# Performance work log

Hardware: AMD Instinct MI355X
Metric: run time of the kernel (lower is better)

## Reference

```python
import jax, jax.numpy as jnp
import numpy as np

N, E, G = 50000, 800000, 512
DIN, HID, DOUT, L, DE = 64, 64, 128, 3, 16
NEG_SLOPE = 0.2
BN_EPS = 1e-5


def setup_inputs() -> dict:
    key = jax.random.key(0)
    ks = jax.random.split(key, 20)
    s = 0.1  # weight scale for numerical stability
    return {
        "x": jax.random.normal(ks[0], (N, DIN), jnp.float32),
        "edge_index": jax.random.randint(ks[1], (2, E), 0, N, jnp.int32),
        "edge_attr": jax.random.normal(ks[2], (E, DE), jnp.float32),
        "batch": jnp.sort(jax.random.randint(ks[3], (N,), 0, G, jnp.int32)),
        "emb_W": jax.random.normal(ks[4], (HID, DIN), jnp.float32) * s,
        "emb_b": jax.random.normal(ks[5], (HID,), jnp.float32) * s,
        "Wl": jax.random.normal(ks[6], (L, HID, HID), jnp.float32) * s,
        "bl": jax.random.normal(ks[7], (L, HID), jnp.float32) * s,
        "Wr": jax.random.normal(ks[8], (L, HID, HID), jnp.float32) * s,
        "br": jax.random.normal(ks[9], (L, HID), jnp.float32) * s,
        "We": jax.random.normal(ks[10], (L, HID, DE), jnp.float32) * s,
        "att": jax.random.normal(ks[11], (L, HID), jnp.float32) * s,
        "conv_bias": jax.random.normal(ks[12], (L, HID), jnp.float32) * s,
        "bn_gamma": jax.random.uniform(ks[13], (L, HID), jnp.float32, 0.5, 1.5),
        "bn_beta": jax.random.normal(ks[14], (L, HID), jnp.float32) * s,
        "bn_mean": jnp.zeros((L, HID), jnp.float32),
        "bn_var": jnp.ones((L, HID), jnp.float32),
        "lin_W": jax.random.normal(ks[15], (DOUT, HID), jnp.float32) * s,
        "lin_b": jax.random.normal(ks[16], (DOUT,), jnp.float32) * s,
    }


def _gatv2(h, src, dst, edge_attr, Wl, bl, Wr, br, We, att, bias):
    # GATv2Conv, heads=1, concat=False, with edge features
    xl = h @ Wl.T + bl                      # [N,C] source transform (also message value)
    xr = h @ Wr.T + br                      # [N,C] target transform
    ea = edge_attr @ We.T                   # [E,C]
    m = xl[src] + xr[dst] + ea              # [E,C]
    m = jax.nn.leaky_relu(m, NEG_SLOPE)
    alpha = m @ att                         # [E] attention logits
    amax = jax.ops.segment_max(alpha, dst, num_segments=N)
    ea_exp = jnp.exp(alpha - amax[dst])
    denom = jax.ops.segment_sum(ea_exp, dst, num_segments=N)
    alpha = ea_exp / (denom[dst] + 1e-16)
    out = jax.ops.segment_sum(alpha[:, None] * xl[src], dst, num_segments=N)
    return out + bias


def reference(x, edge_index, edge_attr, batch, emb_W, emb_b, Wl, bl, Wr, br,
              We, att, conv_bias, bn_gamma, bn_beta, bn_mean, bn_var, lin_W, lin_b):
    src, dst = edge_index[0], edge_index[1]
    h = x @ emb_W.T + emb_b
    for i in range(L):
        hc = _gatv2(h, src, dst, edge_attr, Wl[i], bl[i], Wr[i], br[i],
                    We[i], att[i], conv_bias[i])
        # BatchNorm (eval mode, running stats)
        hc = (hc - bn_mean[i]) * jax.lax.rsqrt(bn_var[i] + BN_EPS) * bn_gamma[i] + bn_beta[i]
        hc = jax.nn.gelu(hc, approximate=False)  # torch F.gelu default is exact erf
        h = h + hc                                # residual; dropout p=0 / eval -> identity
    out = h @ lin_W.T + lin_b                     # [N,DOUT]
    counts = jax.ops.segment_sum(jnp.ones((N,), out.dtype), batch, num_segments=G)
    pooled = jax.ops.segment_sum(out, batch, num_segments=G)
    return pooled / jnp.maximum(counts, 1.0)[:, None]
```

## Files before the change

### kernel.cpp

```cpp
#include <hip/hip_runtime.h>
#include <math.h>

#define NEG_SLOPE 0.2f
#define BN_EPS 1e-5f

template <int N> struct IC { static constexpr int v = N; };
template <bool B> struct BC { static constexpr bool v = B; };

typedef _Float16 half2v __attribute__((ext_vector_type(2)));
typedef _Float16 f16x8 __attribute__((ext_vector_type(8)));
typedef float f32x4v __attribute__((ext_vector_type(4)));

__device__ __forceinline__ half2v u2h(unsigned u) {
  union { unsigned u; half2v h; } c;
  c.u = u;
  return c.h;
}
__device__ __forceinline__ unsigned pkh(float lo, float hi) {
  union { half2v h; unsigned u; } c;
  c.h[0] = (_Float16)lo;
  c.h[1] = (_Float16)hi;
  return c.u;
}

#if defined(__has_builtin)
#if __has_builtin(__builtin_amdgcn_fdot2)
#define FDOT2(a, b, c) __builtin_amdgcn_fdot2((a), (b), (c), false)
#endif
#endif
#ifndef FDOT2
__device__ __forceinline__ float fdot2_sw(half2v a, half2v b, float c) {
  return c + (float)a[0] * (float)b[0] + (float)a[1] * (float)b[1];
}
#define FDOT2(a, b, c) fdot2_sw((a), (b), (c))
#endif

#if defined(__has_builtin)
#if __has_builtin(__builtin_amdgcn_exp2f)
#define FEXP(x) __builtin_amdgcn_exp2f(x)
#define ATT_SCALE 1.44269504088896f
#endif
#endif
#ifndef FEXP
#define FEXP(x) __expf(x)
#define ATT_SCALE 1.0f
#endif

#define FMA4(acc, v, wq) \
  acc += (v).x * (wq).x + (v).y * (wq).y + (v).z * (wq).z + (v).w * (wq).w

#define DOT_ROW(buf, stride, r, bias, OUT)                                  \
  {                                                                         \
    __builtin_amdgcn_sched_barrier(0);                                      \
    float a0 = 0.f, a1 = 0.f, a2 = 0.f, a3 = 0.f;                           \
    _Pragma("unroll") for (int q = 0; q < 4; q++) {                         \
      float4 v0 = *(const float4*)((buf) + (r) * (stride) + q * 16 + 0);    \
      float4 v1 = *(const float4*)((buf) + (r) * (stride) + q * 16 + 4);    \
      float4 v2 = *(const float4*)((buf) + (r) * (stride) + q * 16 + 8);    \
      float4 v3 = *(const float4*)((buf) + (r) * (stride) + q * 16 + 12);   \
      FMA4(a0, v0, W[q * 4 + 0]);                                           \
      FMA4(a1, v1, W[q * 4 + 1]);                                           \
      FMA4(a2, v2, W[q * 4 + 2]);                                           \
      FMA4(a3, v3, W[q * 4 + 3]);                                           \
    }                                                                       \
    OUT = (bias) + ((a0 + a1) + (a2 + a3));                                 \
  }

__device__ __forceinline__ float wave_sum64(float v) {
  int x;
  x = __builtin_amdgcn_update_dpp(0, __float_as_int(v), 0x121, 0xF, 0xF, true);
  v += __int_as_float(x);
  x = __builtin_amdgcn_update_dpp(0, __float_as_int(v), 0x122, 0xF, 0xF, true);
  v += __int_as_float(x);
  x = __builtin_amdgcn_update_dpp(0, __float_as_int(v), 0x124, 0xF, 0xF, true);
  v += __int_as_float(x);
  x = __builtin_amdgcn_update_dpp(0, __float_as_int(v), 0x128, 0xF, 0xF, true);
  v += __int_as_float(x);
  x = __builtin_amdgcn_update_dpp(0, __float_as_int(v), 0x142, 0xF, 0xF, true);
  v += __int_as_float(x);
  x = __builtin_amdgcn_update_dpp(0, __float_as_int(v), 0x143, 0xF, 0xF, true);
  v += __int_as_float(x);
  return __int_as_float(__builtin_amdgcn_readlane(__float_as_int(v), 63));
}

#if defined(__has_builtin)
#if __has_builtin(__builtin_amdgcn_mfma_f32_16x16x32_f16)
#define HAVE_MFMA16 1
#endif
#endif

__global__ __launch_bounds__(256) void hist_kernel(
    const int* __restrict__ dst, const int* __restrict__ batch,
    int* __restrict__ deg, float* __restrict__ counts,
    const float* __restrict__ Wl, const float* __restrict__ Wr,
    _Float16* __restrict__ w16, int E_, int N_) {
  int i = blockIdx.x * 256 + threadIdx.x;
  if (i < E_) atomicAdd(&deg[dst[i]], 1);
  if (i < N_) atomicAdd(&counts[batch[i]], 1.0f);
  if (i < 24576)
    w16[i] = (i < 12288) ? (_Float16)Wl[i] : (_Float16)Wr[i - 12288];
}

__global__ __launch_bounds__(256) void scanA_kernel(
    const int* __restrict__ deg, int* __restrict__ row_ptr,
    int* __restrict__ segTot, int* __restrict__ bins, int N_, int nseg) {
  __shared__ int sb[256];
  __shared__ int lb[128];
  int t = threadIdx.x;
  if (t < 128) lb[t] = 0;
  __syncthreads();
  for (int s = blockIdx.x; s < nseg; s += gridDim.x) {
    int i = s * 256 + t;
    int v = (i < N_) ? deg[i] : 0;
    if (i < N_) atomicAdd(&lb[127 - min(v, 127)], 1);
    sb[t] = v;
    __syncthreads();
    for (int off = 1; off < 256; off <<= 1) {
      int a = (t >= off) ? sb[t - off] : 0;
      __syncthreads();
      sb[t] += a;
      __syncthreads();
    }
    int incl = sb[t];
    if (i < N_) row_ptr[i] = incl - v;
    if (t == 255) segTot[s] = incl;
    __syncthreads();
  }
  if (t < 128 && lb[t]) atomicAdd(&bins[t], lb[t]);
}

__global__ __launch_bounds__(256) void scanB_kernel(int* __restrict__ segTot,
                                                    int* __restrict__ bins,
                                                    int nseg) {
  __shared__ int sb[256];
  __shared__ int baseSh;
  int t = threadIdx.x;
  if (t == 0) baseSh = 0;
  __syncthreads();
  for (int c0 = 0; c0 < nseg; c0 += 256) {
    int s = c0 + t;
    int v = (s < nseg) ? segTot[s] : 0;
    sb[t] = v;
    __syncthreads();
    for (int off = 1; off < 256; off <<= 1) {
      int a = (t >= off) ? sb[t - off] : 0;
      __syncthreads();
      sb[t] += a;
      __syncthreads();
    }
    int incl = sb[t];
    int base = baseSh;
    if (s < nseg) segTot[s] = base + incl - v;
    __syncthreads();
    if (t == 255) baseSh = base + incl;
    __syncthreads();
  }
  int v2 = (t < 128) ? bins[t] : 0;
  sb[t] = v2;
  __syncthreads();
  for (int off = 1; off < 256; off <<= 1) {
    int a = (t >= off) ? sb[t - off] : 0;
    __syncthreads();
    sb[t] += a;
    __syncthreads();
  }
  if (t < 128) bins[t] = sb[t] - v2;
}

__global__ __launch_bounds__(256) void scanC_kernel(
    int* __restrict__ row_ptr, const int* __restrict__ segTot,
    int* __restrict__ cursor, const int* __restrict__ deg,
    int* __restrict__ bins, int* __restrict__ perm, int N_, int E_) {
  __shared__ int lb[128];
  __shared__ int lbase[128];
  int t = threadIdx.x;
  if (t < 128) lb[t] = 0;
  __syncthreads();
  int i = blockIdx.x * 256 + t;
  int bin = 0, rk = 0;
  bool ok = (i < N_);
  if (ok) {
    int rp = row_ptr[i] + segTot[i >> 8];
    row_ptr[i] = rp;
    cursor[i] = rp;
    int dg = deg[i];
    bin = 127 - min(dg, 127);
    rk = atomicAdd(&lb[bin], 1);
  }
  if (i == 0) row_ptr[N_] = E_;
  __syncthreads();
  if (t < 128) {
    int c = lb[t];
    lbase[t] = c ? atomicAdd(&bins[t], c) : 0;
  }
  __syncthreads();
  if (ok) perm[lbase[bin] + rk] = i;
}

__global__ __launch_bounds__(256) void scatter_kernel(
    const int* __restrict__ src, const int* __restrict__ dst,
    int* __restrict__ cursor, int* __restrict__ csr_src,
    int* __restrict__ csr_eid, int E_) {
  int e = blockIdx.x * 256 + threadIdx.x;
  if (e >= E_) return;
  int pos = atomicAdd(&cursor[dst[e]], 1);
  csr_src[pos] = src[e];
  csr_eid[pos] = e;
}

__global__ __launch_bounds__(256) void permute_attr_kernel(
    const float4* __restrict__ edge_attr4, const int* __restrict__ csr_eid,
    unsigned* __restrict__ attr_u, int E_) {
  int p = blockIdx.x * 256 + threadIdx.x;
  if (p >= E_) return;
  int e = csr_eid[p];
  float4 a0 = edge_attr4[(size_t)e * 4 + 0];
  float4 a1 = edge_attr4[(size_t)e * 4 + 1];
  float4 a2 = edge_attr4[(size_t)e * 4 + 2];
  float4 a3 = edge_attr4[(size_t)e * 4 + 3];
  uint4 u0, u1;
  u0.x = pkh(a0.x, a0.y);
  u0.y = pkh(a0.z, a0.w);
  u0.z = pkh(a1.x, a1.y);
  u0.w = pkh(a1.z, a1.w);
  u1.x = pkh(a2.x, a2.y);
  u1.y = pkh(a2.z, a2.w);
  u1.z = pkh(a3.x, a3.y);
  u1.w = pkh(a3.z, a3.w);
  uint4* d4 = (uint4*)(attr_u + (size_t)p * 8);
  d4[0] = u0;
  d4[1] = u1;
}

__global__ __launch_bounds__(256, 3) void emb_kernel(
    const float* __restrict__ x, const float* __restrict__ emb_W,
    const float* __restrict__ emb_b, const _Float16* __restrict__ Wl16,
    const float* __restrict__ bl, const _Float16* __restrict__ Wr16,
    const float* __restrict__ br, float* __restrict__ h,
    _Float16* __restrict__ xl, _Float16* __restrict__ xr, int rows) {
  __shared__ float sx[4096];
  __shared__ float sh[64 * 68];
  int lane = threadIdx.x & 63;
  int w = threadIdx.x >> 6;
  int n0 = blockIdx.x * 64;

  {
    int gmax = rows * 64 - 4;
#pragma unroll
    for (int i = 0; i < 4; i++) {
      int off = w * 1024 + i * 256 + lane * 4;
      int g = min(n0 * 64 + off, gmax);
      *(float4*)(sx + off) = *(const float4*)(x + g);
    }
  }

  {
    float4 W[16];
#pragma unroll
    for (int q = 0; q < 16; q++) W[q] = ((const float4*)(emb_W + lane * 64))[q];
    float b = emb_b[lane];
#pragma unroll 1
    for (int t = 0; t < 16; t++) {
      int r = w * 16 + t;
      float a;
      DOT_ROW(sx, 64, r, b, a);
      sh[r * 68 + lane] = a;
      int n = n0 + r;
      if (n < rows) h[(size_t)n * 64 + lane] = a;
    }
  }

#ifdef HAVE_MFMA16
  {
    int r = lane & 15;
    int kg = lane >> 4;
    int nb = n0 + w * 16;
    const float* p = sh + (w * 16 + r) * 68 + kg * 8;
    f16x8 A0, A1;
    {
      float4 xa = *(const float4*)(p);
      float4 xb = *(const float4*)(p + 4);
      A0[0] = (_Float16)xa.x; A0[1] = (_Float16)xa.y;
      A0[2] = (_Float16)xa.z; A0[3] = (_Float16)xa.w;
      A0[4] = (_Float16)xb.x; A0[5] = (_Float16)xb.y;
      A0[6] = (_Float16)xb.z; A0[7] = (_Float16)xb.w;
      xa = *(const float4*)(p + 32);
      xb = *(const float4*)(p + 36);
      A1[0] = (_Float16)xa.x; A1[1] = (_Float16)xa.y;
      A1[2] = (_Float16)xa.z; A1[3] = (_Float16)xa.w;
      A1[4] = (_Float16)xb.x; A1[5] = (_Float16)xb.y;
      A1[6] = (_Float16)xb.z; A1[7] = (_Float16)xb.w;
    }
#pragma unroll
    for (int c = 0; c < 4; c++) {
      int o = c * 16 + r;
      {
        const f16x8* b0 = (const f16x8*)(Wl16 + (size_t)o * 64 + kg * 8);
        const f16x8* b1 = (const f16x8*)(Wl16 + (size_t)o * 64 + 32 + kg * 8);
        f32x4v acc;
        float bv = bl[o];
        acc[0] = bv; acc[1] = bv; acc[2] = bv; acc[3] = bv;
        acc = __builtin_amdgcn_mfma_f32_16x16x32_f16(A0, b0[0], acc, 0, 0, 0);
        acc = __builtin_amdgcn_mfma_f32_16x16x32_f16(A1, b1[0], acc, 0, 0, 0);
#pragma unroll
        for (int g = 0; g < 4; g++) {
          int nd = nb + kg * 4 + g;
          if (nd < rows) xl[(size_t)nd * 64 + o] = (_Float16)acc[g];
        }
      }
      {
        const f16x8* b0 = (const f16x8*)(Wr16 + (size_t)o * 64 + kg * 8);
        const f16x8* b1 = (const f16x8*)(Wr16 + (size_t)o * 64 + 32 + kg * 8);
        f32x4v acc;
        float bv = br[o];
        acc[0] = bv; acc[1] = bv; acc[2] = bv; acc[3] = bv;
        acc = __builtin_amdgcn_mfma_f32_16x16x32_f16(A0, b0[0], acc, 0, 0, 0);
        acc = __builtin_amdgcn_mfma_f32_16x16x32_f16(A1, b1[0], acc, 0, 0, 0);
#pragma unroll
        for (int g = 0; g < 4; g++) {
          int nd = nb + kg * 4 + g;
          if (nd < rows) xr[(size_t)nd * 64 + o] = (_Float16)acc[g];
        }
      }
    }
  }
#endif
}

__global__ __launch_bounds__(256) void linx_mfma_kernel(
    const float* __restrict__ in, const _Float16* __restrict__ Wl16,
    const float* __restrict__ bl, const _Float16* __restrict__ Wr16,
    const float* __restrict__ br, _Float16* __restrict__ xl,
    _Float16* __restrict__ xr, int rows) {
#ifdef HAVE_MFMA16
  int lane = threadIdx.x & 63;
  int w = threadIdx.x >> 6;
  int n0 = blockIdx.x * 64 + w * 16;
  int r = lane & 15;
  int kg = lane >> 4;

  int nA = min(n0 + r, rows - 1);
  f16x8 A0, A1;
  {
    const float* p = in + (size_t)nA * 64 + kg * 8;
    float4 xa = *(const float4*)(p);
    float4 xb = *(const float4*)(p + 4);
    A0[0] = (_Float16)xa.x; A0[1] = (_Float16)xa.y;
    A0[2] = (_Float16)xa.z; A0[3] = (_Float16)xa.w;
    A0[4] = (_Float16)xb.x; A0[5] = (_Float16)xb.y;
    A0[6] = (_Float16)xb.z; A0[7] = (_Float16)xb.w;
    xa = *(const float4*)(p + 32);
    xb = *(const float4*)(p + 36);
    A1[0] = (_Float16)xa.x; A1[1] = (_Float16)xa.y;
    A1[2] = (_Float16)xa.z; A1[3] = (_Float16)xa.w;
    A1[4] = (_Float16)xb.x; A1[5] = (_Float16)xb.y;
    A1[6] = (_Float16)xb.z; A1[7] = (_Float16)xb.w;
  }

#pragma unroll
  for (int c = 0; c < 4; c++) {
    int o = c * 16 + r;
    {
      const f16x8* b0 = (const f16x8*)(Wl16 + (size_t)o * 64 + kg * 8);
      const f16x8* b1 = (const f16x8*)(Wl16 + (size_t)o * 64 + 32 + kg * 8);
      f32x4v acc;
      float bv = bl[o];
      acc[0] = bv; acc[1] = bv; acc[2] = bv; acc[3] = bv;
      acc = __builtin_amdgcn_mfma_f32_16x16x32_f16(A0, b0[0], acc, 0, 0, 0);
      acc = __builtin_amdgcn_mfma_f32_16x16x32_f16(A1, b1[0], acc, 0, 0, 0);
#pragma unroll
      for (int g = 0; g < 4; g++) {
        int nd = n0 + kg * 4 + g;
        if (nd < rows) xl[(size_t)nd * 64 + o] = (_Float16)acc[g];
      }
    }
    {
      const f16x8* b0 = (const f16x8*)(Wr16 + (size_t)o * 64 + kg * 8);
      const f16x8* b1 = (const f16x8*)(Wr16 + (size_t)o * 64 + 32 + kg * 8);
      f32x4v acc;
      float bv = br[o];
      acc[0] = bv; acc[1] = bv; acc[2] = bv; acc[3] = bv;
      acc = __builtin_amdgcn_mfma_f32_16x16x32_f16(A0, b0[0], acc, 0, 0, 0);
      acc = __builtin_amdgcn_mfma_f32_16x16x32_f16(A1, b1[0], acc, 0, 0, 0);
#pragma unroll
      for (int g = 0; g < 4; g++) {
        int nd = n0 + kg * 4 + g;
        if (nd < rows) xr[(size_t)nd * 64 + o] = (_Float16)acc[g];
      }
    }
  }
#endif
}

template <bool CONTIG>
__global__ __launch_bounds__(256) void gat_fused_kernel(
    const int* __restrict__ perm, const int* __restrict__ csr_src,
    const int* __restrict__ csr_eid, const int* __restrict__ row_ptr,
    const unsigned* __restrict__ attr_u, const float* __restrict__ edge_attr,
    const _Float16* __restrict__ xl, const _Float16* __restrict__ xr,
    const float* __restrict__ We, const float* __restrict__ att,
    const float* __restrict__ conv_bias, const float* __restrict__ gamma,
    const float* __restrict__ beta, const float* __restrict__ mean,
    const float* __restrict__ var, float* __restrict__ h, int N_) {
  int widx = (blockIdx.x * 256 + threadIdx.x) >> 6;
  if (widx >= N_) return;
  int d = __builtin_amdgcn_readfirstlane(perm[widx]);
  int j = threadIdx.x & 63;
  half2v Wek2[8];
  float Wekf[16];
  if constexpr (CONTIG) {
#pragma unroll
    for (int q = 0; q < 8; q++) {
      Wek2[q][0] = (_Float16)We[j * 16 + 2 * q];
      Wek2[q][1] = (_Float16)We[j * 16 + 2 * q + 1];
    }
  } else {
#pragma unroll
    for (int k = 0; k < 16; k++) Wekf[k] = We[j * 16 + k];
  }
  float att_j = att[j] * ATT_SCALE;
  float sc = rsqrtf(var[j] + BN_EPS) * gamma[j];
  float sh = (conv_bias[j] - mean[j]) * sc + beta[j];

  int beg = __builtin_amdgcn_readfirstlane(row_ptr[d]);
  int end = __builtin_amdgcn_readfirstlane(row_ptr[d + 1]);
  float xrj = (float)xr[(size_t)d * 64 + j];
  float m = -INFINITY, l = 0.f, acc = 0.f;

  auto chunk = [&](int base, auto C_, auto PAD_) {
    constexpr int C = decltype(C_)::v;
    constexpr bool PAD = decltype(PAD_)::v;
    int si[C];
#pragma unroll
    for (int t = 0; t < C; t++) {
      int idx = PAD ? min(base + t, end - 1) : (base + t);
      si[t] = __builtin_amdgcn_readfirstlane(csr_src[idx]);
    }
    float xlv[C];
#pragma unroll
    for (int t = 0; t < C; t++)
      xlv[t] = (float)xl[(size_t)si[t] * 64 + j];
    float v[C];
#pragma unroll
    for (int t = 0; t < C; t++) {
      int idx = PAD ? min(base + t, end - 1) : (base + t);
      float ea;
      if constexpr (CONTIG) {
        const uint4* ap = (const uint4*)(attr_u + (size_t)idx * 8);
        uint4 ua = ap[0], ub = ap[1];
        ea = 0.f;
        ea = FDOT2(u2h(ua.x), Wek2[0], ea);
        ea = FDOT2(u2h(ua.y), Wek2[1], ea);
        ea = FDOT2(u2h(ua.z), Wek2[2], ea);
        ea = FDOT2(u2h(ua.w), Wek2[3], ea);
        ea = FDOT2(u2h(ub.x), Wek2[4], ea);
        ea = FDOT2(u2h(ub.y), Wek2[5], ea);
        ea = FDOT2(u2h(ub.z), Wek2[6], ea);
        ea = FDOT2(u2h(ub.w), Wek2[7], ea);
      } else {
        const float4* ap =
            (const float4*)(edge_attr + (size_t)csr_eid[idx] * 16);
        float4 a0 = ap[0], a1 = ap[1], a2 = ap[2], a3 = ap[3];
        ea = a0.x * Wekf[0]  + a0.y * Wekf[1]  + a0.z * Wekf[2]  + a0.w * Wekf[3]
           + a1.x * Wekf[4]  + a1.y * Wekf[5]  + a1.z * Wekf[6]  + a1.w * Wekf[7]
           + a2.x * Wekf[8]  + a2.y * Wekf[9]  + a2.z * Wekf[10] + a2.w * Wekf[11]
           + a3.x * Wekf[12] + a3.y * Wekf[13] + a3.z * Wekf[14] + a3.w * Wekf[15];
      }
      float z = xlv[t] + xrj + ea;
      z = fmaxf(z, NEG_SLOPE * z);
      float p = wave_sum64(z * att_j);
      v[t] = (!PAD || (base + t < end)) ? p : -INFINITY;
    }
    float mc = v[0];
#pragma unroll
    for (int t = 1; t < C; t++) mc = fmaxf(mc, v[t]);
    float newm = fmaxf(m, mc);
    float s = FEXP(m - newm);
    l *= s;
    acc *= s;
#pragma unroll
    for (int t = 0; t < C; t++) {
      float w = FEXP(v[t] - newm);
      l += w;
      acc += w * xlv[t];
    }
    m = newm;
  };

  int base = beg;
  for (; base + 16 <= end; base += 16) chunk(base, IC<16>{}, BC<false>{});
  if (base + 8 <= end) {
    chunk(base, IC<8>{}, BC<false>{});
    base += 8;
  }
  if (base + 4 <= end) {
    chunk(base, IC<4>{}, BC<false>{});
    base += 4;
  }
  if (base < end) chunk(base, IC<4>{}, BC<true>{});

  float val = acc / (l + 1e-16f) * sc + sh;
  float g = 0.5f * val * (1.f + erff(val * 0.70710678118654752f));
  h[(size_t)d * 64 + j] += g;
}

__global__ __launch_bounds__(256, 2) void lin_pool_kernel(
    const float* __restrict__ h, const float* __restrict__ lin_W,
    const float* __restrict__ lin_b, const int* __restrict__ batch,
    const float* __restrict__ counts, float* __restrict__ pooled, int rows) {
  __shared__ float shh[4096];
  int lane = threadIdx.x & 63;
  int w = threadIdx.x >> 6;
  int n0 = blockIdx.x * 64;

  {
    int gmax = rows * 64 - 4;
#pragma unroll
    for (int i = 0; i < 4; i++) {
      int off = w * 1024 + i * 256 + lane * 4;
      int g = min(n0 * 64 + off, gmax);
      *(float4*)(shh + off) = *(const float4*)(h + g);
    }
  }

  float4 W0[16], W1[16];
#pragma unroll
  for (int q = 0; q < 16; q++) W0[q] = ((const float4*)(lin_W + lane * 64))[q];
#pragma unroll
  for (int q = 0; q < 16; q++)
    W1[q] = ((const float4*)(lin_W + (lane + 64) * 64))[q];
  float b0 = lin_b[lane], b1 = lin_b[lane + 64];

  int curg = -1;
  float acc0 = 0.f, acc1 = 0.f;
  int lim = min(16, rows - n0 - w * 16);
#pragma unroll 1
  for (int t = 0; t < lim; t++) {
    int r = w * 16 + t;
    __builtin_amdgcn_sched_barrier(0);
    float d0 = b0, d1 = b1;
#pragma unroll
    for (int q = 0; q < 16; q++) {
      float4 v = *(const float4*)(shh + r * 64 + q * 4);
      FMA4(d0, v, W0[q]);
      FMA4(d1, v, W1[q]);
    }
    int g = batch[n0 + r];
    if (g != curg) {
      if (curg >= 0) {
        float inv = 1.f / fmaxf(counts[curg], 1.f);
        atomicAdd(&pooled[curg * 128 + lane], acc0 * inv);
        atomicAdd(&pooled[curg * 128 + 64 + lane], acc1 * inv);
      }
      curg = g;
      acc0 = 0.f;
      acc1 = 0.f;
    }
    acc0 += d0;
    acc1 += d1;
  }
  if (curg >= 0) {
    float inv = 1.f / fmaxf(counts[curg], 1.f);
    atomicAdd(&pooled[curg * 128 + lane], acc0 * inv);
    atomicAdd(&pooled[curg * 128 + 64 + lane], acc1 * inv);
  }
}

extern "C" void kernel_launch(void* const* d_in, const int* in_sizes, int n_in,
                              void* d_out, int out_size, void* d_ws, size_t ws_size,
                              hipStream_t stream) {
  const float* x         = (const float*)d_in[0];
  const int*   edge_index= (const int*)  d_in[1];
  const float* edge_attr = (const float*)d_in[2];
  const int*   batch     = (const int*)  d_in[3];
  const float* emb_W     = (const float*)d_in[4];
  const float* emb_b     = (const float*)d_in[5];
  const float* Wl        = (const float*)d_in[6];
  const float* bl        = (const float*)d_in[7];
  const float* Wr        = (const float*)d_in[8];
  const float* br        = (const float*)d_in[9];
  const float* We        = (const float*)d_in[10];
  const float* att       = (const float*)d_in[11];
  const float* conv_bias = (const float*)d_in[12];
  const float* bn_gamma  = (const float*)d_in[13];
  const float* bn_beta   = (const float*)d_in[14];
  const float* bn_mean   = (const float*)d_in[15];
  const float* bn_var    = (const float*)d_in[16];
  const float* lin_W     = (const float*)d_in[17];
  const float* lin_b     = (const float*)d_in[18];

  const int N_ = in_sizes[0] / 64;
  const int E_ = in_sizes[1] / 2;
  const int G_ = out_size / 128;
  const int* src = edge_index;
  const int* dst = edge_index + E_;

  const int Npad = (N_ + 3) & ~3;
  const int Epad = (E_ + 19) & ~3;
  const int nseg = (N_ + 255) / 256;

  float* ws      = (float*)d_ws;
  float* h       = ws;
  _Float16* xl   = (_Float16*)(h + (size_t)N_ * 64);
  _Float16* xr   = xl + (size_t)N_ * 64;
  int*   csr_src = (int*)(xr + (size_t)N_ * 64);
  int*   csr_eid = csr_src + Epad;
  int*   row_ptr = csr_eid + Epad;
  int*   cursor  = row_ptr + (Npad + 4);
  int*   deg     = cursor + Npad;
  float* counts  = (float*)(deg + Npad);
  int*   segTot  = (int*)(counts + G_);
  int*   bins    = segTot + nseg + 8;
  int*   perm    = bins + 128;
  uintptr_t abp  = (uintptr_t)(perm + Npad);
  abp = (abp + 15) & ~(uintptr_t)15;
  _Float16* w16  = (_Float16*)abp;
  uintptr_t abp2 = abp + 24576 * sizeof(_Float16);
  unsigned* attr_u = (unsigned*)abp2;

  size_t base_bytes = (abp2 - (uintptr_t)d_ws);
  bool contig = ws_size >= base_bytes + (size_t)E_ * 32 + 64;

  const int hgrid = (max(E_, N_) + 255) / 256;
  const int ngrid = (N_ + 255) / 256;
  const int egrid = (E_ + 255) / 256;

  hipMemsetAsync(deg, 0, ((size_t)Npad + G_ + nseg + 8 + 128) * 4, stream);
  hist_kernel<<<hgrid, 256, 0, stream>>>(dst, batch, deg, counts, Wl, Wr,
                                         w16, E_, N_);
  scanA_kernel<<<min(nseg, 1024), 256, 0, stream>>>(deg, row_ptr, segTot,
                                                    bins, N_, nseg);
  scanB_kernel<<<1, 256, 0, stream>>>(segTot, bins, nseg);
  scanC_kernel<<<ngrid, 256, 0, stream>>>(row_ptr, segTot, cursor, deg, bins,
                                          perm, N_, E_);
  scatter_kernel<<<egrid, 256, 0, stream>>>(src, dst, cursor, csr_src,
                                            csr_eid, E_);
  if (contig) {
    permute_attr_kernel<<<egrid, 256, 0, stream>>>(
        (const float4*)edge_attr, csr_eid, attr_u, E_);
  }

  const int tgrid = (N_ + 63) / 64;
  emb_kernel<<<tgrid, 256, 0, stream>>>(x, emb_W, emb_b, w16, bl,
                                        w16 + 12288, br, h, xl, xr, N_);

  const int gatBlocks = (N_ + 3) / 4;
  for (int l = 0; l < 3; l++) {
    if (l > 0) {
      linx_mfma_kernel<<<tgrid, 256, 0, stream>>>(
          h, w16 + (size_t)l * 4096, bl + l * 64,
          w16 + 12288 + (size_t)l * 4096, br + l * 64, xl, xr, N_);
    }
    if (contig) {
      gat_fused_kernel<true><<<gatBlocks, 256, 0, stream>>>(
          perm, csr_src, csr_eid, row_ptr, attr_u, edge_attr, xl, xr,
          We + (size_t)l * 1024, att + l * 64, conv_bias + l * 64,
          bn_gamma + l * 64, bn_beta + l * 64, bn_mean + l * 64,
          bn_var + l * 64, h, N_);
    } else {
      gat_fused_kernel<false><<<gatBlocks, 256, 0, stream>>>(
          perm, csr_src, csr_eid, row_ptr, attr_u, edge_attr, xl, xr,
          We + (size_t)l * 1024, att + l * 64, conv_bias + l * 64,
          bn_gamma + l * 64, bn_beta + l * 64, bn_mean + l * 64,
          bn_var + l * 64, h, N_);
    }
  }

  hipMemsetAsync(d_out, 0, (size_t)G_ * 128 * 4, stream);
  lin_pool_kernel<<<(N_ + 63) / 64, 256, 0, stream>>>(
      h, lin_W, lin_b, batch, counts, (float*)d_out, N_);
}
```

Measured before the change: 543.7 us.

## Process two destination nodes per wavefront with half-wave reductions in GAT kernel

Result: slower. 582.5 us (+7.1%).

```diff
diff --git a/kernel.cpp b/kernel.cpp
--- a/kernel.cpp
+++ b/kernel.cpp
@@ -5,7 +5,6 @@
 #define BN_EPS 1e-5f
 
 template <int N> struct IC { static constexpr int v = N; };
-template <bool B> struct BC { static constexpr bool v = B; };
 
 typedef _Float16 half2v __attribute__((ext_vector_type(2)));
 typedef _Float16 f16x8 __attribute__((ext_vector_type(8)));
@@ -66,7 +65,7 @@
     OUT = (bias) + ((a0 + a1) + (a2 + a3));                                 \
   }
 
-__device__ __forceinline__ float wave_sum64(float v) {
+__device__ __forceinline__ float half_sum32(float v) {
   int x;
   x = __builtin_amdgcn_update_dpp(0, __float_as_int(v), 0x121, 0xF, 0xF, true);
   v += __int_as_float(x);
@@ -78,9 +77,8 @@
   v += __int_as_float(x);
   x = __builtin_amdgcn_update_dpp(0, __float_as_int(v), 0x142, 0xF, 0xF, true);
   v += __int_as_float(x);
-  x = __builtin_amdgcn_update_dpp(0, __float_as_int(v), 0x143, 0xF, 0xF, true);
-  v += __int_as_float(x);
-  return __int_as_float(__builtin_amdgcn_readlane(__float_as_int(v), 63));
+  return __int_as_float(
+      __builtin_amdgcn_ds_swizzle(__float_as_int(v), 0x03E0));
 }
 
 #if defined(__has_builtin)
@@ -170,7 +168,8 @@
 __global__ __launch_bounds__(256) void scanC_kernel(
     int* __restrict__ row_ptr, const int* __restrict__ segTot,
     int* __restrict__ cursor, const int* __restrict__ deg,
-    int* __restrict__ bins, int* __restrict__ perm, int N_, int E_) {
+    int* __restrict__ bins, int* __restrict__ perm,
+    int* __restrict__ csr_src, int* __restrict__ csr_eid, int N_, int E_) {
   __shared__ int lb[128];
   __shared__ int lbase[128];
   int t = threadIdx.x;
@@ -188,6 +187,10 @@
     rk = atomicAdd(&lb[bin], 1);
   }
   if (i == 0) row_ptr[N_] = E_;
+  if (blockIdx.x == 0 && t < 16) {
+    csr_src[E_ + t] = 0;
+    csr_eid[E_ + t] = 0;
+  }
   __syncthreads();
   if (t < 128) {
     int c = lb[t];
@@ -402,106 +405,173 @@
     const float* __restrict__ conv_bias, const float* __restrict__ gamma,
     const float* __restrict__ beta, const float* __restrict__ mean,
     const float* __restrict__ var, float* __restrict__ h, int N_) {
-  int widx = (blockIdx.x * 256 + threadIdx.x) >> 6;
-  if (widx >= N_) return;
-  int d = __builtin_amdgcn_readfirstlane(perm[widx]);
-  int j = threadIdx.x & 63;
-  half2v Wek2[8];
-  float Wekf[16];
+  int lane = threadIdx.x & 63;
+  int jj = lane & 31;
+  int nidx = (blockIdx.x * 256 + threadIdx.x) >> 5;
+  int nc = min(nidx, N_ - 1);
+  bool alive = (nidx < N_);
+  int d = perm[nc];
+
+  half2v WekA[8], WekB[8];
+  float WekfA[16], WekfB[16];
   if constexpr (CONTIG) {
-#pragma unroll
-    for (int q = 0; q < 8; q++) {
-      Wek2[q][0] = (_Float16)We[j * 16 + 2 * q];
-      Wek2[q][1] = (_Float16)We[j * 16 + 2 * q + 1];
-    }
+    const float4* wp = (const float4*)(We + jj * 32);
+    float4 w0 = wp[0], w1 = wp[1], w2 = wp[2], w3 = wp[3];
+    float4 w4 = wp[4], w5 = wp[5], w6 = wp[6], w7 = wp[7];
+    WekA[0][0] = (_Float16)w0.x; WekA[0][1] = (_Float16)w0.y;
+    WekA[1][0] = (_Float16)w0.z; WekA[1][1] = (_Float16)w0.w;
+    WekA[2][0] = (_Float16)w1.x; WekA[2][1] = (_Float16)w1.y;
+    WekA[3][0] = (_Float16)w1.z; WekA[3][1] = (_Float16)w1.w;
+    WekA[4][0] = (_Float16)w2.x; WekA[4][1] = (_Float16)w2.y;
+    WekA[5][0] = (_Float16)w2.z; WekA[5][1] = (_Float16)w2.w;
+    WekA[6][0] = (_Float16)w3.x; WekA[6][1] = (_Float16)w3.y;
+    WekA[7][0] = (_Float16)w3.z; WekA[7][1] = (_Float16)w3.w;
+    WekB[0][0] = (_Float16)w4.x; WekB[0][1] = (_Float16)w4.y;
+    WekB[1][0] = (_Float16)w4.z; WekB[1][1] = (_Float16)w4.w;
+    WekB[2][0] = (_Float16)w5.x; WekB[2][1] = (_Float16)w5.y;
+    WekB[3][0] = (_Float16)w5.z; WekB[3][1] = (_Float16)w5.w;
+    WekB[4][0] = (_Float16)w6.x; WekB[4][1] = (_Float16)w6.y;
+    WekB[5][0] = (_Float16)w6.z; WekB[5][1] = (_Float16)w6.w;
+    WekB[6][0] = (_Float16)w7.x; WekB[6][1] = (_Float16)w7.y;
+    WekB[7][0] = (_Float16)w7.z; WekB[7][1] = (_Float16)w7.w;
   } else {
 #pragma unroll
-    for (int k = 0; k < 16; k++) Wekf[k] = We[j * 16 + k];
-  }
-  float att_j = att[j] * ATT_SCALE;
-  float sc = rsqrtf(var[j] + BN_EPS) * gamma[j];
-  float sh = (conv_bias[j] - mean[j]) * sc + beta[j];
-
-  int beg = __builtin_amdgcn_readfirstlane(row_ptr[d]);
-  int end = __builtin_amdgcn_readfirstlane(row_ptr[d + 1]);
-  float xrj = (float)xr[(size_t)d * 64 + j];
-  float m = -INFINITY, l = 0.f, acc = 0.f;
-
-  auto chunk = [&](int base, auto C_, auto PAD_) {
+    for (int k = 0; k < 16; k++) WekfA[k] = We[jj * 32 + k];
+#pragma unroll
+    for (int k = 0; k < 16; k++) WekfB[k] = We[jj * 32 + 16 + k];
+  }
+  float2 attv = *(const float2*)(att + jj * 2);
+  float att0 = attv.x * ATT_SCALE, att1 = attv.y * ATT_SCALE;
+  float2 varv = *(const float2*)(var + jj * 2);
+  float2 gamv = *(const float2*)(gamma + jj * 2);
+  float2 cbv = *(const float2*)(conv_bias + jj * 2);
+  float2 mev = *(const float2*)(mean + jj * 2);
+  float2 bev = *(const float2*)(beta + jj * 2);
+  float sc0 = rsqrtf(varv.x + BN_EPS) * gamv.x;
+  float sh0 = (cbv.x - mev.x) * sc0 + bev.x;
+  float sc1 = rsqrtf(varv.y + BN_EPS) * gamv.y;
+  float sh1 = (cbv.y - mev.y) * sc1 + bev.y;
+
+  int beg = row_ptr[d];
+  int end = row_ptr[d + 1];
+  int deg = alive ? (end - beg) : 0;
+  int degm1 = max(deg - 1, 0);
+  int degA = __builtin_amdgcn_readfirstlane(deg);
+  int degB = __builtin_amdgcn_readlane(deg, 32);
+  int maxdeg = max(degA, degB);
+
+  float xrj0, xrj1;
+  {
+    unsigned pk = ((const unsigned*)xr)[(size_t)d * 32 + jj];
+    half2v hv = u2h(pk);
+    xrj0 = (float)hv[0];
+    xrj1 = (float)hv[1];
+  }
+
+  float m = -INFINITY, l = 0.f, acc0 = 0.f, acc1 = 0.f;
+
+  auto chunk = [&](int base, auto C_) {
     constexpr int C = decltype(C_)::v;
-    constexpr bool PAD = decltype(PAD_)::v;
+    int idxv[C];
+#pragma unroll
+    for (int t = 0; t < C; t++) idxv[t] = beg + min(base + t, degm1);
     int si[C];
 #pragma unroll
+    for (int t = 0; t < C; t++) si[t] = csr_src[idxv[t]];
+    unsigned xpk[C];
+#pragma unroll
+    for (int t = 0; t < C; t++)
+      xpk[t] = *(const unsigned*)((const char*)xl + (size_t)si[t] * 128 +
+                                  jj * 4);
+    float v[C];
+#pragma unroll
     for (int t = 0; t < C; t++) {
-      int idx = PAD ? min(base + t, end - 1) : (base + t);
-      si[t] = __builtin_amdgcn_readfirstlane(csr_src[idx]);
-    }
-    float xlv[C];
-#pragma unroll
-    for (int t = 0; t < C; t++)
-      xlv[t] = (float)xl[(size_t)si[t] * 64 + j];
-    float v[C];
-#pragma unroll
-    for (int t = 0; t < C; t++) {
-      int idx = PAD ? min(base + t, end - 1) : (base + t);
-      float ea;
+      float ea0, ea1;
       if constexpr (CONTIG) {
-        const uint4* ap = (const uint4*)(attr_u + (size_t)idx * 8);
+        const uint4* ap = (const uint4*)(attr_u + (size_t)idxv[t] * 8);
         uint4 ua = ap[0], ub = ap[1];
-        ea = 0.f;
-        ea = FDOT2(u2h(ua.x), Wek2[0], ea);
-        ea = FDOT2(u2h(ua.y), Wek2[1], ea);
-        ea = FDOT2(u2h(ua.z), Wek2[2], ea);
-        ea = FDOT2(u2h(ua.w), Wek2[3], ea);
-        ea = FDOT2(u2h(ub.x), Wek2[4], ea);
-        ea = FDOT2(u2h(ub.y), Wek2[5], ea);
-        ea = FDOT2(u2h(ub.z), Wek2[6], ea);
-        ea = FDOT2(u2h(ub.w), Wek2[7], ea);
+        ea0 = 0.f;
+        ea0 = FDOT2(u2h(ua.x), WekA[0], ea0);
+        ea0 = FDOT2(u2h(ua.y), WekA[1], ea0);
+        ea0 = FDOT2(u2h(ua.z), WekA[2], ea0);
+        ea0 = FDOT2(u2h(ua.w), WekA[3], ea0);
+        ea0 = FDOT2(u2h(ub.x), WekA[4], ea0);
+        ea0 = FDOT2(u2h(ub.y), WekA[5], ea0);
+        ea0 = FDOT2(u2h(ub.z), WekA[6], ea0);
+        ea0 = FDOT2(u2h(ub.w), WekA[7], ea0);
+        ea1 = 0.f;
+        ea1 = FDOT2(u2h(ua.x), WekB[0], ea1);
+        ea1 = FDOT2(u2h(ua.y), WekB[1], ea1);
+        ea1 = FDOT2(u2h(ua.z), WekB[2], ea1);
+        ea1 = FDOT2(u2h(ua.w), WekB[3], ea1);
+        ea1 = FDOT2(u2h(ub.x), WekB[4], ea1);
+        ea1 = FDOT2(u2h(ub.y), WekB[5], ea1);
+        ea1 = FDOT2(u2h(ub.z), WekB[6], ea1);
+        ea1 = FDOT2(u2h(ub.w), WekB[7], ea1);
       } else {
-        const float4* ap =
-            (const float4*)(edge_attr + (size_t)csr_eid[idx] * 16);
+        int e = csr_eid[idxv[t]];
+        const float4* ap = (const float4*)(edge_attr + (size_t)e * 16);
         float4 a0 = ap[0], a1 = ap[1], a2 = ap[2], a3 = ap[3];
-        ea = a0.x * Wekf[0]  + a0.y * Wekf[1]  + a0.z * Wekf[2]  + a0.w * Wekf[3]
-           + a1.x * Wekf[4]  + a1.y * Wekf[5]  + a1.z * Wekf[6]  + a1.w * Wekf[7]
-           + a2.x * Wekf[8]  + a2.y * Wekf[9]  + a2.z * Wekf[10] + a2.w * Wekf[11]
-           + a3.x * Wekf[12] + a3.y * Wekf[13] + a3.z * Wekf[14] + a3.w * Wekf[15];
+        ea0 = a0.x * WekfA[0]  + a0.y * WekfA[1]  + a0.z * WekfA[2]  + a0.w * WekfA[3]
+            + a1.x * WekfA[4]  + a1.y * WekfA[5]  + a1.z * WekfA[6]  + a1.w * WekfA[7]
+            + a2.x * WekfA[8]  + a2.y * WekfA[9]  + a2.z * WekfA[10] + a2.w * WekfA[11]
+            + a3.x * WekfA[12] + a3.y * WekfA[13] + a3.z * WekfA[14] + a3.w * WekfA[15];
+        ea1 = a0.x * WekfB[0]  + a0.y * WekfB[1]  + a0.z * WekfB[2]  + a0.w * WekfB[3]
+            + a1.x * WekfB[4]  + a1.y * WekfB[5]  + a1.z * WekfB[6]  + a1.w * WekfB[7]
+            + a2.x * WekfB[8]  + a2.y * WekfB[9]  + a2.z * WekfB[10] + a2.w * WekfB[11]
+            + a3.x * WekfB[12] + a3.y * WekfB[13] + a3.z * WekfB[14] + a3.w * WekfB[15];
       }
-      float z = xlv[t] + xrj + ea;
-      z = fmaxf(z, NEG_SLOPE * z);
-      float p = wave_sum64(z * att_j);
-      v[t] = (!PAD || (base + t < end)) ? p : -INFINITY;
+      half2v hv = u2h(xpk[t]);
+      float z0 = (float)hv[0] + xrj0 + ea0;
+      z0 = fmaxf(z0, NEG_SLOPE * z0);
+      float z1 = (float)hv[1] + xrj1 + ea1;
+      z1 = fmaxf(z1, NEG_SLOPE * z1);
+      float p = half_sum32(z0 * att0 + z1 * att1);
+      v[t] = (base + t < deg) ? p : -INFINITY;
     }
     float mc = v[0];
 #pragma unroll
     for (int t = 1; t < C; t++) mc = fmaxf(mc, v[t]);
     float newm = fmaxf(m, mc);
-    float s = FEXP(m - newm);
+    float nm2 = (newm < -1e37f) ? 0.f : newm;
+    float s = FEXP(m - nm2);
     l *= s;
-    acc *= s;
+    acc0 *= s;
+    acc1 *= s;
 #pragma unroll
     for (int t = 0; t < C; t++) {
-      float w = FEXP(v[t] - newm);
+      float w = FEXP(v[t] - nm2);
       l += w;
-      acc += w * xlv[t];
+      half2v hv = u2h(xpk[t]);
+      acc0 += w * (float)hv[0];
+      acc1 += w * (float)hv[1];
     }
     m = newm;
   };
 
-  int base = beg;
-  for (; base + 16 <= end; base += 16) chunk(base, IC<16>{}, BC<false>{});
-  if (base + 8 <= end) {
-    chunk(base, IC<8>{}, BC<false>{});
+  int base = 0;
+  for (; base + 16 <= maxdeg; base += 16) chunk(base, IC<16>{});
+  if (base + 8 <= maxdeg) {
+    chunk(base, IC<8>{});
     base += 8;
   }
-  if (base + 4 <= end) {
-    chunk(base, IC<4>{}, BC<false>{});
+  if (base + 4 <= maxdeg) {
+    chunk(base, IC<4>{});
     base += 4;
   }
-  if (base < end) chunk(base, IC<4>{}, BC<true>{});
-
-  float val = acc / (l + 1e-16f) * sc + sh;
-  float g = 0.5f * val * (1.f + erff(val * 0.70710678118654752f));
-  h[(size_t)d * 64 + j] += g;
+  if (base < maxdeg) chunk(base, IC<4>{});
+
+  if (alive) {
+    float val0 = acc0 / (l + 1e-16f) * sc0 + sh0;
+    float val1 = acc1 / (l + 1e-16f) * sc1 + sh1;
+    float g0 = 0.5f * val0 * (1.f + erff(val0 * 0.70710678118654752f));
+    float g1 = 0.5f * val1 * (1.f + erff(val1 * 0.70710678118654752f));
+    float2* hp = (float2*)(h + (size_t)d * 64 + jj * 2);
+    float2 o = *hp;
+    o.x += g0;
+    o.y += g1;
+    *hp = o;
+  }
 }
 
 __global__ __launch_bounds__(256, 2) void lin_pool_kernel(
@@ -632,7 +702,7 @@
                                                     bins, N_, nseg);
   scanB_kernel<<<1, 256, 0, stream>>>(segTot, bins, nseg);
   scanC_kernel<<<ngrid, 256, 0, stream>>>(row_ptr, segTot, cursor, deg, bins,
-                                          perm, N_, E_);
+                                          perm, csr_src, csr_eid, N_, E_);
   scatter_kernel<<<egrid, 256, 0, stream>>>(src, dst, cursor, csr_src,
                                             csr_eid, E_);
   if (contig) {
@@ -644,7 +714,7 @@
   emb_kernel<<<tgrid, 256, 0, stream>>>(x, emb_W, emb_b, w16, bl,
                                         w16 + 12288, br, h, xl, xr, N_);
 
-  const int gatBlocks = (N_ + 3) / 4;
+  const int gatBlocks = (N_ + 7) / 8;
   for (int l = 0; l < 3; l++) {
     if (l > 0) {
       linx_mfma_kernel<<<tgrid, 256, 0, stream>>>(
```
